# Kernel tuning notes

Measured on AMD Instinct MI355X. Metric: run time of the kernel, lower is better.

The kernel has to match this reference:

```python
import jax, jax.numpy as jnp
import numpy as np

D_L = 64
HIDDEN = 64
CUBE = (D_L + 1) ** 3  # 274625


def setup_inputs() -> dict:
    key = jax.random.key(0)
    ks = jax.random.split(key, 9)
    B = 512
    l = jax.random.normal(ks[0], (B, D_L), dtype=jnp.float32)
    a = jax.random.normal(ks[1], (B, D_L), dtype=jnp.float32)
    v = jax.random.normal(ks[2], (B, D_L), dtype=jnp.float32)
    # Linear params (xavier-ish scale)
    W1 = jax.random.normal(ks[3], (CUBE, HIDDEN), dtype=jnp.float32) * (1.0 / np.sqrt(CUBE))
    b1 = jnp.zeros((HIDDEN,), dtype=jnp.float32)
    W2 = jax.random.normal(ks[4], (HIDDEN, HIDDEN), dtype=jnp.float32) * (1.0 / np.sqrt(HIDDEN))
    b2 = jnp.zeros((HIDDEN,), dtype=jnp.float32)
    W3 = jax.random.normal(ks[5], (HIDDEN, D_L), dtype=jnp.float32) * (1.0 / np.sqrt(HIDDEN))
    b3 = jnp.zeros((D_L,), dtype=jnp.float32)
    return {"l": l, "a": a, "v": v, "W1": W1, "b1": b1, "W2": W2, "b2": b2, "W3": W3, "b3": b3}


def reference(l, a, v, W1, b1, W2, b2, W3, b3):
    B = a.shape[0]
    ones = jnp.ones((B, 1), dtype=a.dtype)
    a_h = jnp.concatenate([ones, a], axis=1)  # [B, d+1]
    v_h = jnp.concatenate([ones, v], axis=1)
    t_h = jnp.concatenate([ones, l], axis=1)
    # fusion[b, i, j, k] = a_h[b,i] * v_h[b,j] * t_h[b,k]; flattened row-major (i,j,k)
    fusion = jnp.einsum('bi,bj,bk->bijk', a_h, v_h, t_h).reshape(B, -1)  # [B, (d+1)^3]
    h = jnp.tanh(fusion @ W1 + b1)
    h = jnp.tanh(h @ W2 + b2)
    out = jnp.tanh(h @ W3 + b3)
    return out
```

## Files before the change

### kernel.cpp

```cpp
#include <hip/hip_runtime.h>
#include <hip/hip_fp16.h>


typedef _Float16 f16;
typedef f16 f16x8 __attribute__((ext_vector_type(8)));
typedef f16 f16x2 __attribute__((ext_vector_type(2)));
typedef __fp16 fp16x2 __attribute__((ext_vector_type(2)));
typedef float fx4 __attribute__((ext_vector_type(4)));

#define WS_AT    0
#define WS_VT    131072
#define WS_PART  262144

__device__ __forceinline__ f16x2 pkrtz(float a, float b) {
  fp16x2 r = __builtin_amdgcn_cvt_pkrtz(a, b);
  return *(f16x2*)&r;
}

__device__ __forceinline__ void seg_decode(int s, int& ia, int& iv, int& isel,
                                           int& rowbase, int& rowstride) {
  if (s < 4096)      { int i = s >> 6, j = s & 63; ia = i; iv = j; isel = 0;
                       rowbase = (i+1)*4225 + (j+1)*65 + 1; rowstride = 1; }
  else if (s < 4160) { int i = s - 4096; ia = i; iv = -1; isel = 2;
                       rowbase = (i+1)*4225 + 65; rowstride = 65; }
  else if (s < 4224) { int i = s - 4160; ia = i; iv = -1; isel = 0;
                       rowbase = (i+1)*4225 + 1; rowstride = 1; }
  else if (s < 4288) { int j = s - 4224; ia = -1; iv = j; isel = 0;
                       rowbase = (j+1)*65 + 1; rowstride = 1; }
  else if (s == 4288){ ia = -1; iv = -1; isel = 1; rowbase = 4225; rowstride = 4225; }
  else if (s == 4289){ ia = -1; iv = -1; isel = 2; rowbase = 65;   rowstride = 65; }
  else if (s == 4290){ ia = -1; iv = -1; isel = 0; rowbase = 1;    rowstride = 1; }
  else               { ia = -2; iv = -1; isel = 0; rowbase = 1;    rowstride = 1; }
}

__device__ __forceinline__ f16x8 cvt8(fx4 x0, fx4 x1) {
  f16x8 f;
  f[0]=(f16)x0[0]; f[1]=(f16)x0[1]; f[2]=(f16)x0[2]; f[3]=(f16)x0[3];
  f[4]=(f16)x1[0]; f[5]=(f16)x1[1]; f[6]=(f16)x1[2]; f[7]=(f16)x1[3];
  return f;
}

__global__ __launch_bounds__(256) void prep_kernel(
    const float* __restrict__ a, const float* __restrict__ v,
    float* __restrict__ aT, float* __restrict__ vT)
{
  int g = blockIdx.x * 256 + threadIdx.x;
  int which = g >> 15;
  int idx = g & 32767;
  if (which == 0) aT[idx] = a[((idx & 511) << 6) + (idx >> 9)];
  else            vT[idx] = v[((idx & 511) << 6) + (idx >> 9)];
}

__global__ __launch_bounds__(256, 2) void fusion_gemm(
    const float* __restrict__ W1,
    const float* __restrict__ aT, const float* __restrict__ vT,
    const float* __restrict__ a, const float* __restrict__ v, const float* __restrict__ l,
    f16* __restrict__ partials)
{
  __shared__ f16 pl_all[17][256];

  const int tid  = threadIdx.x;
  const int bid  = blockIdx.x;
  const int grp  = bid >> 4;
  const int rr   = bid & 15;
  const int half = rr >> 3;
  const int slot = rr & 7;
  const int chunk = (grp << 3) + slot;
  const int lane = tid & 63;
  const int wave = tid >> 6;
  const int l15  = lane & 15;
  const int l4   = lane >> 4;
  const int segbase = chunk * 17;
  const int row0 = half << 8;

  #pragma unroll
  for (int t = 0; t < 17; ++t) {
    int s = segbase + t, ia, iv, is_, rb, rs;
    seg_decode(s, ia, iv, is_, rb, rs);
    float spa = (ia >= 0) ? aT[(ia << 9) + row0 + tid] : (ia == -1 ? 1.0f : 0.0f);
    float spv = (iv >= 0) ? vT[(iv << 9) + row0 + tid] : 1.0f;
    pl_all[t][tid] = (f16)(spa * spv);
  }

  f16x8 lfrag[4][2], vfrag[4][2];
  #pragma unroll
  for (int mt = 0; mt < 4; ++mt) {
    int row = row0 + (wave << 6) + (mt << 4) + l15;
    #pragma unroll
    for (int ks = 0; ks < 2; ++ks) {
      const float* pl_ = l + (row << 6) + (ks << 5) + (l4 << 3);
      lfrag[mt][ks] = cvt8(*(const fx4*)pl_, *(const fx4*)(pl_ + 4));
      const float* pv_ = v + (row << 6) + (ks << 5) + (l4 << 3);
      vfrag[mt][ks] = cvt8(*(const fx4*)pv_, *(const fx4*)(pv_ + 4));
    }
  }

  fx4 acc[4][4] = {};

  __syncthreads();

  #pragma unroll 1
  for (int t = 0; t < 17; ++t) {
    int s = segbase + t, ia_, iv_, isel, rb, rs;
    seg_decode(s, ia_, iv_, isel, rb, rs);

    f16x8 av[4][2];
    #pragma unroll
    for (int mt = 0; mt < 4; ++mt) {
      int lrow = (wave << 6) + (mt << 4) + l15;
      f16 ps = pl_all[t][lrow];
      f16x2 ps2 = { ps, ps };
      #pragma unroll
      for (int ks = 0; ks < 2; ++ks) {
        f16x8 lv;
        if (isel == 0)      lv = lfrag[mt][ks];
        else if (isel == 2) lv = vfrag[mt][ks];
        else { const float* p_ = a + ((size_t)(row0 + lrow) << 6) + (ks << 5) + (l4 << 3);
               lv = cvt8(*(const fx4*)p_, *(const fx4*)(p_ + 4)); }
        ((f16x2*)&av[mt][ks])[0] = ((f16x2*)&lv)[0] * ps2;
        ((f16x2*)&av[mt][ks])[1] = ((f16x2*)&lv)[1] * ps2;
        ((f16x2*)&av[mt][ks])[2] = ((f16x2*)&lv)[2] * ps2;
        ((f16x2*)&av[mt][ks])[3] = ((f16x2*)&lv)[3] * ps2;
      }
    }

    float w[2][4][8];
    if (rs == 1) {
      const float* b0 = W1 + (((size_t)(rb + (l4 << 3))) << 6) + l15;
      const float* b1 = b0 + (32 << 6);
      #pragma unroll
      for (int nt = 0; nt < 4; ++nt)
        #pragma unroll
        for (int e = 0; e < 8; ++e) {
          w[0][nt][e] = b0[(nt << 4) + (e << 6)];
          w[1][nt][e] = b1[(nt << 4) + (e << 6)];
        }
    } else {
      #pragma unroll
      for (int ks = 0; ks < 2; ++ks)
        #pragma unroll
        for (int nt = 0; nt < 4; ++nt) {
          const float* b = W1 + (size_t)(rb + ((ks << 5) + (l4 << 3)) * rs) * 64 + (nt << 4) + l15;
          #pragma unroll
          for (int e = 0; e < 8; ++e) w[ks][nt][e] = b[(size_t)(e * rs) << 6];
        }
    }

    #pragma unroll
    for (int ks = 0; ks < 2; ++ks)
      #pragma unroll
      for (int nt = 0; nt < 4; ++nt) {
        f16x8 bf;
        ((f16x2*)&bf)[0] = pkrtz(w[ks][nt][0], w[ks][nt][1]);
        ((f16x2*)&bf)[1] = pkrtz(w[ks][nt][2], w[ks][nt][3]);
        ((f16x2*)&bf)[2] = pkrtz(w[ks][nt][4], w[ks][nt][5]);
        ((f16x2*)&bf)[3] = pkrtz(w[ks][nt][6], w[ks][nt][7]);
        #pragma unroll
        for (int mt = 0; mt < 4; ++mt)
          acc[mt][nt] = __builtin_amdgcn_mfma_f32_16x16x32_f16(av[mt][ks], bf, acc[mt][nt], 0, 0, 0);
      }
  }

  #pragma unroll
  for (int mt = 0; mt < 4; ++mt)
    #pragma unroll
    for (int nt = 0; nt < 4; ++nt)
      #pragma unroll
      for (int r = 0; r < 4; ++r) {
        int grow = row0 + (wave << 6) + (mt << 4) + (l4 << 2) + r;
        int col = (nt << 4) + l15;
        partials[((size_t)grow << 14) + (chunk << 6) + col] = (f16)acc[mt][nt][r];
      }
}

__global__ __launch_bounds__(256) void tail_kernel(
    const f16* __restrict__ partials, const float* __restrict__ W1, const float* __restrict__ b1,
    const float* __restrict__ W2, const float* __restrict__ b2,
    const float* __restrict__ W3, const float* __restrict__ b3, float* __restrict__ out)
{
  __shared__ float red[256][8];
  __shared__ float hbuf[64];
  __shared__ float h2buf[64];
  const int row = blockIdx.x;
  const int t = threadIdx.x;
  const f16* base = partials + ((size_t)row << 14);

  float s[8] = {0.f,0.f,0.f,0.f,0.f,0.f,0.f,0.f};
  #pragma unroll
  for (int j = 0; j < 8; ++j) {
    f16x8 vv = *(const f16x8*)(base + (((j << 8) + t) << 3));
    #pragma unroll
    for (int e = 0; e < 8; ++e) s[e] += (float)vv[e];
  }
  #pragma unroll
  for (int e = 0; e < 8; ++e) red[t][e] = s[e];
  __syncthreads();
  if (t < 64) {
    float acc = b1[t] + W1[t];
    #pragma unroll
    for (int k = 0; k < 32; ++k) acc += red[(t >> 3) + (k << 3)][t & 7];
    hbuf[t] = tanhf(acc);
  }
  __syncthreads();
  if (t < 64) {
    float acc = b2[t];
    #pragma unroll 8
    for (int k = 0; k < 64; ++k) acc += hbuf[k] * W2[(k << 6) + t];
    h2buf[t] = tanhf(acc);
  }
  __syncthreads();
  if (t < 64) {
    float acc = b3[t];
    #pragma unroll 8
    for (int k = 0; k < 64; ++k) acc += h2buf[k] * W3[(k << 6) + t];
    out[(row << 6) + t] = tanhf(acc);
  }
}

extern "C" void kernel_launch(void* const* d_in, const int* in_sizes, int n_in,
                              void* d_out, int out_size, void* d_ws, size_t ws_size,
                              hipStream_t stream) {
  const float* l  = (const float*)d_in[0];
  const float* a  = (const float*)d_in[1];
  const float* v  = (const float*)d_in[2];
  const float* W1 = (const float*)d_in[3];
  const float* b1 = (const float*)d_in[4];
  const float* W2 = (const float*)d_in[5];
  const float* b2 = (const float*)d_in[6];
  const float* W3 = (const float*)d_in[7];
  const float* b3 = (const float*)d_in[8];
  float* out = (float*)d_out;

  char* ws = (char*)d_ws;
  float* aT = (float*)(ws + WS_AT);
  float* vT = (float*)(ws + WS_VT);
  f16* partials = (f16*)(ws + WS_PART);

  hipLaunchKernelGGL(prep_kernel, dim3(256), dim3(256), 0, stream, a, v, aT, vT);
  hipLaunchKernelGGL(fusion_gemm, dim3(512), dim3(256), 0, stream,
                     W1, aT, vT, a, v, l, partials);
  hipLaunchKernelGGL(tail_kernel, dim3(512), dim3(256), 0, stream,
                     partials, W1, b1, W2, b2, W3, b3, out);
}
```

Before: 73.81 us.

## Re-tile fusion GEMM by N per wave, double-buffer W1 loads, rebalance chunks

Each block now handles 128 rows, and each wave owns one 16-column N slice across eight M tiles, so a wave loads only its own slice of W1 per segment. W1 loads are double-buffered in registers: the next segment's loads are issued before the current segment's MFMAs, to hide global-memory latency. The segment space is re-split into 192 chunks of 23 segments over 768 blocks, with occupancy raised to 3 blocks per CU. In exchange, the a and v fragments are re-read from global memory on the rare segments that need them, more blocks share the same activation rows, and register pressure changes under the tighter launch bound.

```diff
diff --git a/kernel.cpp b/kernel.cpp
--- a/kernel.cpp
+++ b/kernel.cpp
@@ -8,6 +8,8 @@
 typedef __fp16 fp16x2 __attribute__((ext_vector_type(2)));
 typedef float fx4 __attribute__((ext_vector_type(4)));
 
+#define NCHUNK 192
+#define NSEG   23
 #define WS_AT    0
 #define WS_VT    131072
 #define WS_PART  262144
@@ -51,126 +53,135 @@
   else            vT[idx] = v[((idx & 511) << 6) + (idx >> 9)];
 }
 
-__global__ __launch_bounds__(256, 2) void fusion_gemm(
+__global__ __launch_bounds__(256, 3) void fusion_gemm(
     const float* __restrict__ W1,
     const float* __restrict__ aT, const float* __restrict__ vT,
     const float* __restrict__ a, const float* __restrict__ v, const float* __restrict__ l,
     f16* __restrict__ partials)
 {
-  __shared__ f16 pl_all[17][256];
+  __shared__ f16 pl_all[NSEG][128];
 
   const int tid  = threadIdx.x;
   const int bid  = blockIdx.x;
-  const int grp  = bid >> 4;
-  const int rr   = bid & 15;
-  const int half = rr >> 3;
-  const int slot = rr & 7;
-  const int chunk = (grp << 3) + slot;
+  const int cLo  = bid & 7;
+  const int q    = bid >> 3;
+  const int mg   = q & 3;
+  const int chunk= ((q >> 2) << 3) + cLo;
   const int lane = tid & 63;
   const int wave = tid >> 6;
   const int l15  = lane & 15;
   const int l4   = lane >> 4;
-  const int segbase = chunk * 17;
-  const int row0 = half << 8;
-
-  #pragma unroll
-  for (int t = 0; t < 17; ++t) {
-    int s = segbase + t, ia, iv, is_, rb, rs;
-    seg_decode(s, ia, iv, is_, rb, rs);
-    float spa = (ia >= 0) ? aT[(ia << 9) + row0 + tid] : (ia == -1 ? 1.0f : 0.0f);
-    float spv = (iv >= 0) ? vT[(iv << 9) + row0 + tid] : 1.0f;
-    pl_all[t][tid] = (f16)(spa * spv);
-  }
-
-  f16x8 lfrag[4][2], vfrag[4][2];
-  #pragma unroll
-  for (int mt = 0; mt < 4; ++mt) {
-    int row = row0 + (wave << 6) + (mt << 4) + l15;
+  const int segbase = chunk * NSEG;
+  const int row0 = mg << 7;
+  const int n0   = (wave << 4) + l15;
+
+  if (tid < 128) {
+    #pragma unroll
+    for (int t = 0; t < NSEG; ++t) {
+      int s = segbase + t, ia, iv, is_, rb, rs;
+      seg_decode(s, ia, iv, is_, rb, rs);
+      float spa = (ia >= 0) ? aT[(ia << 9) + row0 + tid] : (ia == -1 ? 1.0f : 0.0f);
+      float spv = (iv >= 0) ? vT[(iv << 9) + row0 + tid] : 1.0f;
+      pl_all[t][tid] = (f16)(spa * spv);
+    }
+  }
+
+  f16x8 lfrag[8][2];
+  #pragma unroll
+  for (int mt = 0; mt < 8; ++mt) {
+    int row = row0 + (mt << 4) + l15;
     #pragma unroll
     for (int ks = 0; ks < 2; ++ks) {
-      const float* pl_ = l + (row << 6) + (ks << 5) + (l4 << 3);
-      lfrag[mt][ks] = cvt8(*(const fx4*)pl_, *(const fx4*)(pl_ + 4));
-      const float* pv_ = v + (row << 6) + (ks << 5) + (l4 << 3);
-      vfrag[mt][ks] = cvt8(*(const fx4*)pv_, *(const fx4*)(pv_ + 4));
+      const float* p = l + ((size_t)row << 6) + (ks << 5) + (l4 << 3);
+      lfrag[mt][ks] = cvt8(*(const fx4*)p, *(const fx4*)(p + 4));
     }
   }
 
-  fx4 acc[4][4] = {};
-
-  __syncthreads();
-
+  fx4 acc[8] = {};
+
+  __syncthreads();
+
+  float w[2][2][8];
+
+#define ISSUE(SL, T) do {                                                     \
+    int s_ = segbase + (T), ia_, iv_, is_, rb_, rs_;                          \
+    seg_decode(s_, ia_, iv_, is_, rb_, rs_);                                  \
+    if (rs_ == 1) {                                                           \
+      const float* b0_ = W1 + (((size_t)(rb_ + (l4 << 3))) << 6) + n0;        \
+      const float* b1_ = b0_ + 2048;                                          \
+      _Pragma("unroll")                                                       \
+      for (int e_ = 0; e_ < 8; ++e_) {                                        \
+        w[SL][0][e_] = b0_[e_ << 6];                                          \
+        w[SL][1][e_] = b1_[e_ << 6];                                          \
+      }                                                                       \
+    } else {                                                                  \
+      _Pragma("unroll")                                                       \
+      for (int ks_ = 0; ks_ < 2; ++ks_)                                       \
+        _Pragma("unroll")                                                     \
+        for (int e_ = 0; e_ < 8; ++e_) {                                      \
+          int k_ = (ks_ << 5) + (l4 << 3) + e_;                               \
+          w[SL][ks_][e_] = W1[((size_t)(rb_ + k_ * rs_) << 6) + n0];          \
+        }                                                                     \
+    }                                                                         \
+  } while (0)
+
+#define CONSUME(SL, T) do {                                                   \
+    int s_ = segbase + (T);                                                   \
+    int isel_ = ((s_ >= 4096 && s_ < 4160) || s_ == 4289) ? 2                 \
+              : (s_ == 4288 ? 1 : 0);                                         \
+    f16x8 bf0_, bf1_;                                                         \
+    ((f16x2*)&bf0_)[0] = pkrtz(w[SL][0][0], w[SL][0][1]);                     \
+    ((f16x2*)&bf0_)[1] = pkrtz(w[SL][0][2], w[SL][0][3]);                     \
+    ((f16x2*)&bf0_)[2] = pkrtz(w[SL][0][4], w[SL][0][5]);                     \
+    ((f16x2*)&bf0_)[3] = pkrtz(w[SL][0][6], w[SL][0][7]);                     \
+    ((f16x2*)&bf1_)[0] = pkrtz(w[SL][1][0], w[SL][1][1]);                     \
+    ((f16x2*)&bf1_)[1] = pkrtz(w[SL][1][2], w[SL][1][3]);                     \
+    ((f16x2*)&bf1_)[2] = pkrtz(w[SL][1][4], w[SL][1][5]);                     \
+    ((f16x2*)&bf1_)[3] = pkrtz(w[SL][1][6], w[SL][1][7]);                     \
+    _Pragma("unroll")                                                         \
+    for (int mt_ = 0; mt_ < 8; ++mt_) {                                       \
+      f16 ps_ = pl_all[T][(mt_ << 4) + l15];                                  \
+      f16x2 ps2_ = { ps_, ps_ };                                              \
+      _Pragma("unroll")                                                       \
+      for (int ks_ = 0; ks_ < 2; ++ks_) {                                     \
+        f16x8 lv_;                                                            \
+        if (isel_ == 0) lv_ = lfrag[mt_][ks_];                                \
+        else {                                                                \
+          const float* p_ = (isel_ == 1 ? a : v)                              \
+              + ((size_t)(row0 + (mt_ << 4) + l15) << 6) + (ks_ << 5) + (l4 << 3); \
+          lv_ = cvt8(*(const fx4*)p_, *(const fx4*)(p_ + 4));                 \
+        }                                                                     \
+        f16x8 av_;                                                            \
+        ((f16x2*)&av_)[0] = ((f16x2*)&lv_)[0] * ps2_;                         \
+        ((f16x2*)&av_)[1] = ((f16x2*)&lv_)[1] * ps2_;                         \
+        ((f16x2*)&av_)[2] = ((f16x2*)&lv_)[2] * ps2_;                         \
+        ((f16x2*)&av_)[3] = ((f16x2*)&lv_)[3] * ps2_;                         \
+        acc[mt_] = __builtin_amdgcn_mfma_f32_16x16x32_f16(                    \
+            av_, (ks_ == 0 ? bf0_ : bf1_), acc[mt_], 0, 0, 0);                \
+      }                                                                       \
+    }                                                                         \
+  } while (0)
+
+  ISSUE(0, 0);
   #pragma unroll 1
-  for (int t = 0; t < 17; ++t) {
-    int s = segbase + t, ia_, iv_, isel, rb, rs;
-    seg_decode(s, ia_, iv_, isel, rb, rs);
-
-    f16x8 av[4][2];
-    #pragma unroll
-    for (int mt = 0; mt < 4; ++mt) {
-      int lrow = (wave << 6) + (mt << 4) + l15;
-      f16 ps = pl_all[t][lrow];
-      f16x2 ps2 = { ps, ps };
-      #pragma unroll
-      for (int ks = 0; ks < 2; ++ks) {
-        f16x8 lv;
-        if (isel == 0)      lv = lfrag[mt][ks];
-        else if (isel == 2) lv = vfrag[mt][ks];
-        else { const float* p_ = a + ((size_t)(row0 + lrow) << 6) + (ks << 5) + (l4 << 3);
-               lv = cvt8(*(const fx4*)p_, *(const fx4*)(p_ + 4)); }
-        ((f16x2*)&av[mt][ks])[0] = ((f16x2*)&lv)[0] * ps2;
-        ((f16x2*)&av[mt][ks])[1] = ((f16x2*)&lv)[1] * ps2;
-        ((f16x2*)&av[mt][ks])[2] = ((f16x2*)&lv)[2] * ps2;
-        ((f16x2*)&av[mt][ks])[3] = ((f16x2*)&lv)[3] * ps2;
-      }
+  for (int p = 0; p < 11; ++p) {
+    const int t2 = p * 2;
+    ISSUE(1, t2 + 1);
+    CONSUME(0, t2);
+    ISSUE(0, t2 + 2);
+    CONSUME(1, t2 + 1);
+  }
+  CONSUME(0, 22);
+#undef ISSUE
+#undef CONSUME
+
+  #pragma unroll
+  for (int mt = 0; mt < 8; ++mt)
+    #pragma unroll
+    for (int r = 0; r < 4; ++r) {
+      int grow = row0 + (mt << 4) + (l4 << 2) + r;
+      partials[(size_t)grow * (NCHUNK * 64) + (chunk << 6) + n0] = (f16)acc[mt][r];
     }
-
-    float w[2][4][8];
-    if (rs == 1) {
-      const float* b0 = W1 + (((size_t)(rb + (l4 << 3))) << 6) + l15;
-      const float* b1 = b0 + (32 << 6);
-      #pragma unroll
-      for (int nt = 0; nt < 4; ++nt)
-        #pragma unroll
-        for (int e = 0; e < 8; ++e) {
-          w[0][nt][e] = b0[(nt << 4) + (e << 6)];
-          w[1][nt][e] = b1[(nt << 4) + (e << 6)];
-        }
-    } else {
-      #pragma unroll
-      for (int ks = 0; ks < 2; ++ks)
-        #pragma unroll
-        for (int nt = 0; nt < 4; ++nt) {
-          const float* b = W1 + (size_t)(rb + ((ks << 5) + (l4 << 3)) * rs) * 64 + (nt << 4) + l15;
-          #pragma unroll
-          for (int e = 0; e < 8; ++e) w[ks][nt][e] = b[(size_t)(e * rs) << 6];
-        }
-    }
-
-    #pragma unroll
-    for (int ks = 0; ks < 2; ++ks)
-      #pragma unroll
-      for (int nt = 0; nt < 4; ++nt) {
-        f16x8 bf;
-        ((f16x2*)&bf)[0] = pkrtz(w[ks][nt][0], w[ks][nt][1]);
-        ((f16x2*)&bf)[1] = pkrtz(w[ks][nt][2], w[ks][nt][3]);
-        ((f16x2*)&bf)[2] = pkrtz(w[ks][nt][4], w[ks][nt][5]);
-        ((f16x2*)&bf)[3] = pkrtz(w[ks][nt][6], w[ks][nt][7]);
-        #pragma unroll
-        for (int mt = 0; mt < 4; ++mt)
-          acc[mt][nt] = __builtin_amdgcn_mfma_f32_16x16x32_f16(av[mt][ks], bf, acc[mt][nt], 0, 0, 0);
-      }
-  }
-
-  #pragma unroll
-  for (int mt = 0; mt < 4; ++mt)
-    #pragma unroll
-    for (int nt = 0; nt < 4; ++nt)
-      #pragma unroll
-      for (int r = 0; r < 4; ++r) {
-        int grow = row0 + (wave << 6) + (mt << 4) + (l4 << 2) + r;
-        int col = (nt << 4) + l15;
-        partials[((size_t)grow << 14) + (chunk << 6) + col] = (f16)acc[mt][nt][r];
-      }
 }
 
 __global__ __launch_bounds__(256) void tail_kernel(
@@ -183,11 +194,11 @@
   __shared__ float h2buf[64];
   const int row = blockIdx.x;
   const int t = threadIdx.x;
-  const f16* base = partials + ((size_t)row << 14);
+  const f16* base = partials + (size_t)row * (NCHUNK * 64);
 
   float s[8] = {0.f,0.f,0.f,0.f,0.f,0.f,0.f,0.f};
   #pragma unroll
-  for (int j = 0; j < 8; ++j) {
+  for (int j = 0; j < 6; ++j) {
     f16x8 vv = *(const f16x8*)(base + (((j << 8) + t) << 3));
     #pragma unroll
     for (int e = 0; e < 8; ++e) s[e] += (float)vv[e];
@@ -237,7 +248,7 @@
   f16* partials = (f16*)(ws + WS_PART);
 
   hipLaunchKernelGGL(prep_kernel, dim3(256), dim3(256), 0, stream, a, v, aT, vT);
-  hipLaunchKernelGGL(fusion_gemm, dim3(512), dim3(256), 0, stream,
+  hipLaunchKernelGGL(fusion_gemm, dim3(768), dim3(256), 0, stream,
                      W1, aT, vT, a, v, l, partials);
   hipLaunchKernelGGL(tail_kernel, dim3(512), dim3(256), 0, stream,
                      partials, W1, b1, W2, b2, W3, b3, out);
```

Result: slower. 161.2 us (+118.4%).
